# Kernel optimization log

Measured on AMD Instinct MI355X. Metric: run time of the kernel, lower is better.

## Reference

```python
import jax, jax.numpy as jnp
import numpy as np

N, E, NG = 10000, 160000, 64
HID, HEADS = 256, 4
NEG_SLOPE = 0.2


def setup_inputs() -> dict:
    key = jax.random.key(0)
    ks = jax.random.split(key, 20)
    s = 0.1
    inp = {
        "atom_features": jax.random.normal(ks[0], (N, 23), jnp.float32),
        "edge_index": jax.random.randint(ks[1], (2, E), 0, N),
        "batch": jnp.sort(jax.random.randint(ks[2], (N,), 0, NG)),
        "W1": jax.random.normal(ks[3], (23, HEADS * HID), jnp.float32) * s,
        "as1": jax.random.normal(ks[4], (HEADS, HID), jnp.float32) * s,
        "ad1": jax.random.normal(ks[5], (HEADS, HID), jnp.float32) * s,
        "b1": jnp.zeros((HEADS * HID,), jnp.float32),
        "W2": jax.random.normal(ks[6], (HEADS * HID, HEADS * HID), jnp.float32) * s,
        "as2": jax.random.normal(ks[7], (HEADS, HID), jnp.float32) * s,
        "ad2": jax.random.normal(ks[8], (HEADS, HID), jnp.float32) * s,
        "b2": jnp.zeros((HEADS * HID,), jnp.float32),
        "W3": jax.random.normal(ks[9], (HEADS * HID, HID), jnp.float32) * s,
        "as3": jax.random.normal(ks[10], (1, HID), jnp.float32) * s,
        "ad3": jax.random.normal(ks[11], (1, HID), jnp.float32) * s,
        "b3": jnp.zeros((HID,), jnp.float32),
        # MLP head
        "fc1_w": jax.random.normal(ks[12], (HID, HID // 2), jnp.float32) * s,
        "fc1_b": jnp.zeros((HID // 2,), jnp.float32),
        "fc2_w": jax.random.normal(ks[13], (HID // 2, 1), jnp.float32) * s,
        "fc2_b": jnp.zeros((1,), jnp.float32),
    }
    return inp


def gat_layer(x, W, att_src, att_dst, bias, src, dst, heads, ch):
    n = x.shape[0]
    h = (x @ W).reshape(n, heads, ch)                      # [N,H,C]
    a_s = jnp.sum(h * att_src, axis=-1)                    # [N,H]
    a_d = jnp.sum(h * att_dst, axis=-1)                    # [N,H]
    logits = jax.nn.leaky_relu(a_s[src] + a_d[dst], NEG_SLOPE)  # [E',H]
    m = jax.ops.segment_max(logits, dst, num_segments=n)
    m = jnp.where(jnp.isfinite(m), m, 0.0)
    e = jnp.exp(logits - m[dst])
    denom = jax.ops.segment_sum(e, dst, num_segments=n)
    alpha = e / (denom[dst] + 1e-16)                       # segment softmax over incoming edges
    out = jax.ops.segment_sum(alpha[:, :, None] * h[src], dst, num_segments=n)
    return out.reshape(n, heads * ch) + bias


def reference(atom_features, edge_index, batch,
              W1, as1, ad1, b1, W2, as2, ad2, b2, W3, as3, ad3, b3,
              fc1_w, fc1_b, fc2_w, fc2_b):
    n = atom_features.shape[0]
    loops = jnp.arange(n)
    src = jnp.concatenate([edge_index[0], loops])   # PyG GATConv adds self-loops
    dst = jnp.concatenate([edge_index[1], loops])

    x = jax.nn.elu(gat_layer(atom_features, W1, as1, ad1, b1, src, dst, HEADS, HID))
    x = jax.nn.elu(gat_layer(x, W2, as2, ad2, b2, src, dst, HEADS, HID))
    x = jax.nn.elu(gat_layer(x, W3, as3, ad3, b3, src, dst, 1, HID))
    # dropout: eval mode (training=False) -> identity

    # global mean pool over molecules
    sums = jax.ops.segment_sum(x, batch, num_segments=NG)
    counts = jax.ops.segment_sum(jnp.ones((n,), x.dtype), batch, num_segments=NG)
    features = sums / jnp.maximum(counts, 1.0)[:, None]    # [NG, HID]

    hmid = jax.nn.relu(features @ fc1_w + fc1_b)
    validity = hmid @ fc2_w + fc2_b                        # [NG, 1]
    return validity, features
```

## Files before the change

kernel.cpp:

```cpp
#include <hip/hip_runtime.h>
#include <hip/hip_bf16.h>
#include <math.h>

typedef unsigned short ushortT;
typedef __attribute__((ext_vector_type(8))) short short8;
typedef __attribute__((ext_vector_type(4))) float f32x4;

constexpr int NN   = 10000;
constexpr int EE   = 160000;
constexpr int ETOT = EE + NN;
constexpr int NG   = 64;
constexpr int HID  = 256;
constexpr int HEADS = 4;

__device__ __forceinline__ ushortT f2bf(float x) {
    __hip_bfloat16 h = __float2bfloat16(x);
    return *reinterpret_cast<ushortT*>(&h);
}
__device__ __forceinline__ float bf2f(ushortT x) {
    unsigned u = ((unsigned)x) << 16;
    return __uint_as_float(u);
}

__device__ __forceinline__ int xcd_swz(int flat, int nwg) {
    int q = nwg >> 3, r = nwg & 7;
    int xcd = flat & 7, j = flat >> 3;
    return (xcd < r ? xcd * (q + 1) : r * (q + 1) + (xcd - r) * q) + j;
}

__global__ void edge_count_kernel(const int* __restrict__ ei, int* __restrict__ cnt) {
    int e = blockIdx.x * blockDim.x + threadIdx.x;
    if (e >= ETOT) return;
    int dst = (e < EE) ? ei[EE + e] : (e - EE);
    atomicAdd(&cnt[dst], 1);
}

__global__ void scan_kernel(const int* __restrict__ cnt, int* __restrict__ row_ptr,
                            int* __restrict__ cursor) {
    __shared__ int part[256];
    int tid = threadIdx.x;
    const int chunk = (NN + 255) / 256;
    int s0 = tid * chunk;
    int s1 = min(NN, s0 + chunk);
    int sum = 0;
    for (int i = s0; i < s1; ++i) sum += cnt[i];
    part[tid] = sum;
    __syncthreads();
    for (int off = 1; off < 256; off <<= 1) {
        int v = (tid >= off) ? part[tid - off] : 0;
        __syncthreads();
        part[tid] += v;
        __syncthreads();
    }
    int run = (tid == 0) ? 0 : part[tid - 1];
    for (int i = s0; i < s1; ++i) {
        row_ptr[i] = run;
        cursor[i]  = run;
        run += cnt[i];
    }
    if (tid == 255) row_ptr[NN] = part[255];
}

__global__ void edge_fill_kernel(const int* __restrict__ ei, int* __restrict__ cursor,
                                 int* __restrict__ col_src) {
    int e = blockIdx.x * blockDim.x + threadIdx.x;
    if (e >= ETOT) return;
    int src, dst;
    if (e < EE) { src = ei[e]; dst = ei[EE + e]; }
    else        { src = dst = e - EE; }
    int pos = atomicAdd(&cursor[dst], 1);
    col_src[pos] = src;
}

__global__ void convert_wt2(const float* __restrict__ W2, ushortT* __restrict__ wt2,
                            const float* __restrict__ W3, ushortT* __restrict__ wt3) {
    const float* W; ushortT* Wt; int N;
    if (blockIdx.z == 0) { W = W2; Wt = wt2; N = 1024; }
    else                 { W = W3; Wt = wt3; N = 256; if (blockIdx.x >= 8) return; }
    const int K = 1024, Kp = 1024;
    __shared__ float t[32][33];
    int n0 = blockIdx.x * 32, k0 = blockIdx.y * 32;
    int tx = threadIdx.x, ty = threadIdx.y;
    for (int i = ty; i < 32; i += 8) {
        int k = k0 + i, n = n0 + tx;
        t[i][tx] = (k < K && n < N) ? W[(size_t)k * N + n] : 0.f;
    }
    __syncthreads();
    for (int i = ty; i < 32; i += 8) {
        int n = n0 + i, kp = k0 + tx;
        if (n < N && kp < Kp) Wt[(size_t)n * Kp + kp] = f2bf(t[tx][i]);
    }
}

__global__ void build_b1p(const float* __restrict__ W1, ushortT* __restrict__ Bp) {
    int idx = blockIdx.x * 256 + threadIdx.x;
    if (idx >= 1024 * 128) return;
    int n = idx >> 7, kp = idx & 127;
    int h = n >> 8, hk = kp >> 5, k = kp & 31;
    float v = (hk == h && k < 23) ? W1[(size_t)k * 1024 + n] : 0.f;
    Bp[idx] = f2bf(v);
}

__global__ void proj_all(const float* __restrict__ W1, const float* __restrict__ as1,
                         const float* __restrict__ ad1, float* __restrict__ wsv1,
                         const float* __restrict__ W2, const float* __restrict__ as2,
                         const float* __restrict__ ad2, float* __restrict__ wsv2,
                         const float* __restrict__ W3, const float* __restrict__ as3,
                         const float* __restrict__ ad3, float* __restrict__ wsv3) {
    int gw   = (blockIdx.x * 256 + threadIdx.x) >> 6;
    int lane = threadIdx.x & 63;
    const float *W, *atts, *attd; float* wsv; int heads, idx;
    if (gw < 23 * 8)               { W = W1; atts = as1; attd = ad1; wsv = wsv1; heads = 4; idx = gw; }
    else if (gw < 23 * 8 + 8192)   { W = W2; atts = as2; attd = ad2; wsv = wsv2; heads = 4; idx = gw - 184; }
    else if (gw < 23 * 8 + 8192 + 2048) { W = W3; atts = as3; attd = ad3; wsv = wsv3; heads = 1; idx = gw - 184 - 8192; }
    else return;
    const int nout = 2 * heads;
    int k = idx / nout, o = idx - k * nout;
    int h = (o >= heads) ? (o - heads) : o;
    const float* att  = ((o >= heads) ? attd : atts) + h * HID;
    const float* wrow = W + (size_t)k * (heads * HID) + h * HID;
    float4 w4 = *(const float4*)(wrow + lane * 4);
    float4 a4 = *(const float4*)(att + lane * 4);
    float s = w4.x * a4.x + w4.y * a4.y + w4.z * a4.z + w4.w * a4.w;
    #pragma unroll
    for (int off = 1; off < 64; off <<= 1) s += __shfl_xor(s, off);
    if (lane == 0) wsv[(size_t)k * nout + o] = s;
}

__global__ void dots1_kernel(const float* __restrict__ atom,
                             const float* __restrict__ wsv1,
                             float* __restrict__ a_s, float* __restrict__ a_d) {
    int n = blockIdx.x * 256 + threadIdx.x;
    if (n >= NN) return;
    float a[8] = {0.f, 0.f, 0.f, 0.f, 0.f, 0.f, 0.f, 0.f};
    #pragma unroll
    for (int k = 0; k < 23; ++k) {
        float x = atom[n * 23 + k];
        #pragma unroll
        for (int o = 0; o < 8; ++o) a[o] += x * wsv1[k * 8 + o];
    }
    #pragma unroll
    for (int h = 0; h < 4; ++h) { a_s[n * 4 + h] = a[h]; a_d[n * 4 + h] = a[4 + h]; }
}

__global__ void dots2_kernel(const ushortT* __restrict__ x,
                             const float* __restrict__ wsv,
                             float* __restrict__ a_s, float* __restrict__ a_d) {
    int gw = (blockIdx.x * 256 + threadIdx.x) >> 6;
    int lane = threadIdx.x & 63;
    if (gw >= NN) return;
    const ushortT* row = x + (size_t)gw * 1024 + lane * 16;
    short8 v0 = *(const short8*)row;
    short8 v1 = *(const short8*)(row + 8);
    float ps[8] = {0.f, 0.f, 0.f, 0.f, 0.f, 0.f, 0.f, 0.f};
    const float* wb = wsv + (size_t)lane * 16 * 8;
    #pragma unroll
    for (int c = 0; c < 8; ++c) {
        float xv = bf2f((ushortT)v0[c]);
        #pragma unroll
        for (int o = 0; o < 8; ++o) ps[o] += xv * wb[c * 8 + o];
    }
    #pragma unroll
    for (int c = 0; c < 8; ++c) {
        float xv = bf2f((ushortT)v1[c]);
        #pragma unroll
        for (int o = 0; o < 8; ++o) ps[o] += xv * wb[(8 + c) * 8 + o];
    }
    #pragma unroll
    for (int off = 1; off < 64; off <<= 1) {
        #pragma unroll
        for (int o = 0; o < 8; ++o) ps[o] += __shfl_xor(ps[o], off);
    }
    if (lane == 0) {
        #pragma unroll
        for (int h = 0; h < 4; ++h) { a_s[gw * 4 + h] = ps[h]; a_d[gw * 4 + h] = ps[4 + h]; }
    }
}

__global__ void dots3_kernel(const ushortT* __restrict__ x,
                             const float* __restrict__ wsv,
                             float* __restrict__ a_s, float* __restrict__ a_d) {
    int gw = (blockIdx.x * 256 + threadIdx.x) >> 6;
    int lane = threadIdx.x & 63;
    if (gw >= NN) return;
    const ushortT* row = x + (size_t)gw * 1024 + lane * 16;
    short8 v0 = *(const short8*)row;
    short8 v1 = *(const short8*)(row + 8);
    float p0 = 0.f, p1 = 0.f;
    const int c0 = lane * 16;
    #pragma unroll
    for (int c = 0; c < 8; ++c) {
        float xv = bf2f((ushortT)v0[c]);
        float2 w2 = *(const float2*)(wsv + (size_t)(c0 + c) * 2);
        p0 += xv * w2.x; p1 += xv * w2.y;
    }
    #pragma unroll
    for (int c = 0; c < 8; ++c) {
        float xv = bf2f((ushortT)v1[c]);
        float2 w2 = *(const float2*)(wsv + (size_t)(c0 + 8 + c) * 2);
        p0 += xv * w2.x; p1 += xv * w2.y;
    }
    #pragma unroll
    for (int off = 1; off < 64; off <<= 1) {
        p0 += __shfl_xor(p0, off);
        p1 += __shfl_xor(p1, off);
    }
    if (lane == 0) { a_s[gw] = p0; a_d[gw] = p1; }
}

__global__ __launch_bounds__(256) void agg_atom_kernel(const float* __restrict__ atom,
                                                       const float* __restrict__ a_s,
                                                       const float* __restrict__ a_d,
                                                       const int* __restrict__ rowp,
                                                       const int* __restrict__ colv,
                                                       ushortT* __restrict__ Ap) {
    const int wv = threadIdx.x >> 6, lane = threadIdx.x & 63;
    const int i = blockIdx.x * 4 + wv;
    if (i >= NN) return;
    const int half = lane >> 5, c = lane & 31;
    const int start = rowp[i], end = rowp[i + 1];

    __shared__ float wsh[4][64][4];
    __shared__ int   ssh[4][64];

    float acc[4] = {0.f, 0.f, 0.f, 0.f};
    float den4[4] = {0.f, 0.f, 0.f, 0.f};
    for (int cb = start; cb < end; cb += 64) {
        int clen = min(64, end - cb);
        if (lane < clen) {
            int s = colv[cb + lane];
            ssh[wv][lane] = s;
            float4 as4 = *(const float4*)(a_s + (size_t)s * 4);
            float4 ad4 = *(const float4*)(a_d + (size_t)i * 4);
            float l0 = as4.x + ad4.x; l0 = (l0 >= 0.f) ? l0 : 0.2f * l0;
            float l1 = as4.y + ad4.y; l1 = (l1 >= 0.f) ? l1 : 0.2f * l1;
            float l2 = as4.z + ad4.z; l2 = (l2 >= 0.f) ? l2 : 0.2f * l2;
            float l3 = as4.w + ad4.w; l3 = (l3 >= 0.f) ? l3 : 0.2f * l3;
            float w0 = expf(l0), w1 = expf(l1), w2 = expf(l2), w3 = expf(l3);
            *reinterpret_cast<float4*>(&wsh[wv][lane][0]) = make_float4(w0, w1, w2, w3);
            den4[0] += w0; den4[1] += w1; den4[2] += w2; den4[3] += w3;
        }
        __builtin_amdgcn_wave_barrier();
        for (int e = half; e < clen; e += 2) {
            int s = ssh[wv][e];
            float x = (c < 23) ? atom[(size_t)s * 23 + c] : 0.f;
            acc[0] += wsh[wv][e][0] * x;
            acc[1] += wsh[wv][e][1] * x;
            acc[2] += wsh[wv][e][2] * x;
            acc[3] += wsh[wv][e][3] * x;
        }
        __builtin_amdgcn_wave_barrier();
    }
    #pragma unroll
    for (int h = 0; h < 4; ++h) acc[h] += __shfl_xor(acc[h], 32);
    #pragma unroll
    for (int off = 1; off < 64; off <<= 1) {
        den4[0] += __shfl_xor(den4[0], off);
        den4[1] += __shfl_xor(den4[1], off);
        den4[2] += __shfl_xor(den4[2], off);
        den4[3] += __shfl_xor(den4[3], off);
    }
    if (half == 0) {
        #pragma unroll
        for (int h = 0; h < 4; ++h) {
            float v = acc[h] / (den4[h] + 1e-16f);
            Ap[(size_t)i * 128 + h * 32 + c] = f2bf(v);
        }
    }
}

__device__ __forceinline__ void gload_lds16(const ushortT* gsrc, ushortT* ldst) {
    __builtin_amdgcn_global_load_lds(
        (const __attribute__((address_space(1))) unsigned int*)gsrc,
        (__attribute__((address_space(3))) unsigned int*)ldst, 16, 0, 0);
}

template<int MODE>
__global__ __launch_bounds__(256, 2) void gemm_bf16(const ushortT* __restrict__ A,
                                                    const ushortT* __restrict__ Bt,
                                                    ushortT* __restrict__ C,
                                                    const float* __restrict__ bias,
                                                    int M, int N, int K) {
    __shared__ ushortT lds[2][2][128][32];
    const int tid  = threadIdx.x;
    const int lane = tid & 63, w = tid >> 6;
    const int wm = w >> 1, wn = w & 1;
    const int nwg  = gridDim.x * gridDim.y;
    const int flat = blockIdx.y * gridDim.x + blockIdx.x;
    const int swz  = xcd_swz(flat, nwg);
    const int bx = swz % gridDim.x, by = swz / gridDim.x;
    const int row0 = by * 128;
    const int col0 = bx * 128;
    const int nt = K >> 5;

    auto stage = [&](int buf, int t) {
        int k0 = t << 5;
        #pragma unroll
        for (int i = 0; i < 2; ++i) {
            int gbase = (w * 2 + i) * 64;
            int g = gbase + lane;
            int row = g >> 2;
            int sw = (row & 3) ^ ((row >> 2) & 3);
            int koff = (g & 3) ^ sw;
            int arow = min(row0 + row, M - 1);
            gload_lds16(A + (size_t)arow * K + k0 + koff * 8,
                        &lds[buf][0][0][0] + gbase * 8);
            int brow = col0 + row;
            gload_lds16(Bt + (size_t)brow * K + k0 + koff * 8,
                        &lds[buf][1][0][0] + gbase * 8);
        }
    };

    f32x4 acc[4][4] = {};
    const int lr = lane & 15, lk = lane >> 4;

    stage(0, 0);
    for (int t = 0; t < nt; ++t) {
        int buf = t & 1;
        __syncthreads();
        if (t + 1 < nt) stage(buf ^ 1, t + 1);
        short8 a[4], b[4];
        const ushortT* baseA = &lds[buf][0][0][0];
        const ushortT* baseB = &lds[buf][1][0][0];
        #pragma unroll
        for (int m = 0; m < 4; ++m) {
            int row = wm * 64 + m * 16 + lr;
            int sw = (row & 3) ^ ((row >> 2) & 3);
            a[m] = *(const short8*)(baseA + row * 32 + ((lk ^ sw) * 8));
        }
        #pragma unroll
        for (int n = 0; n < 4; ++n) {
            int row = wn * 64 + n * 16 + lr;
            int sw = (row & 3) ^ ((row >> 2) & 3);
            b[n] = *(const short8*)(baseB + row * 32 + ((lk ^ sw) * 8));
        }
        #pragma unroll
        for (int m = 0; m < 4; ++m)
            #pragma unroll
            for (int n = 0; n < 4; ++n)
                acc[m][n] = __builtin_amdgcn_mfma_f32_16x16x32_bf16(a[m], b[n], acc[m][n], 0, 0, 0);
    }

    #pragma unroll
    for (int m = 0; m < 4; ++m) {
        #pragma unroll
        for (int n = 0; n < 4; ++n) {
            int col = col0 + wn * 64 + n * 16 + lr;
            float bv = (MODE == 1) ? bias[col] : 0.f;
            #pragma unroll
            for (int j = 0; j < 4; ++j) {
                int rowg = row0 + wm * 64 + m * 16 + lk * 4 + j;
                if (rowg < M) {
                    float v = acc[m][n][j];
                    if (MODE == 1) { v += bv; v = (v > 0.f) ? v : expm1f(v); }
                    C[(size_t)rowg * N + col] = f2bf(v);
                }
            }
        }
    }
}

__global__ __launch_bounds__(256) void gat_agg_h4(const ushortT* __restrict__ hfeat,
                                                  const float* __restrict__ a_s,
                                                  const float* __restrict__ a_d,
                                                  const int* __restrict__ rowp,
                                                  const int* __restrict__ colv,
                                                  const float* __restrict__ bias,
                                                  ushortT* __restrict__ out16) {
    const int wv = threadIdx.x >> 6, lane = threadIdx.x & 63;
    const int i = blockIdx.x * 4 + wv;
    if (i >= NN) return;
    const int c0 = lane * 16;
    const int hh = c0 >> 8;
    const int start = rowp[i], end = rowp[i + 1];

    __shared__ float wsh[4][64][4];
    __shared__ int   ssh[4][64];

    float acc[16];
    #pragma unroll
    for (int c = 0; c < 16; ++c) acc[c] = 0.f;
    float den4[4] = {0.f, 0.f, 0.f, 0.f};

    for (int cb = start; cb < end; cb += 64) {
        int clen = min(64, end - cb);
        if (lane < clen) {
            int s = colv[cb + lane];
            ssh[wv][lane] = s;
            float4 as4 = *(const float4*)(a_s + (size_t)s * 4);
            float4 ad4 = *(const float4*)(a_d + (size_t)i * 4);
            float l0 = as4.x + ad4.x; l0 = (l0 >= 0.f) ? l0 : 0.2f * l0;
            float l1 = as4.y + ad4.y; l1 = (l1 >= 0.f) ? l1 : 0.2f * l1;
            float l2 = as4.z + ad4.z; l2 = (l2 >= 0.f) ? l2 : 0.2f * l2;
            float l3 = as4.w + ad4.w; l3 = (l3 >= 0.f) ? l3 : 0.2f * l3;
            float w0 = expf(l0), w1 = expf(l1), w2 = expf(l2), w3 = expf(l3);
            *reinterpret_cast<float4*>(&wsh[wv][lane][0]) = make_float4(w0, w1, w2, w3);
            den4[0] += w0; den4[1] += w1; den4[2] += w2; den4[3] += w3;
        }
        __builtin_amdgcn_wave_barrier();
        int e = 0;
        for (; e + 4 <= clen; e += 4) {
            int sa = ssh[wv][e], sb = ssh[wv][e + 1], sc = ssh[wv][e + 2], sd = ssh[wv][e + 3];
            const ushortT* pa = hfeat + (size_t)sa * 1024 + c0;
            const ushortT* pb = hfeat + (size_t)sb * 1024 + c0;
            const ushortT* pc = hfeat + (size_t)sc * 1024 + c0;
            const ushortT* pd = hfeat + (size_t)sd * 1024 + c0;
            short8 va0 = *(const short8*)pa,       va1 = *(const short8*)(pa + 8);
            short8 vb0 = *(const short8*)pb,       vb1 = *(const short8*)(pb + 8);
            short8 vc0 = *(const short8*)pc,       vc1 = *(const short8*)(pc + 8);
            short8 vd0 = *(const short8*)pd,       vd1 = *(const short8*)(pd + 8);
            float wa = wsh[wv][e][hh],     wb = wsh[wv][e + 1][hh];
            float wc = wsh[wv][e + 2][hh], wd = wsh[wv][e + 3][hh];
            #pragma unroll
            for (int j = 0; j < 8; ++j) {
                acc[j]     += wa * bf2f((ushortT)va0[j]) + wb * bf2f((ushortT)vb0[j])
                            + wc * bf2f((ushortT)vc0[j]) + wd * bf2f((ushortT)vd0[j]);
                acc[8 + j] += wa * bf2f((ushortT)va1[j]) + wb * bf2f((ushortT)vb1[j])
                            + wc * bf2f((ushortT)vc1[j]) + wd * bf2f((ushortT)vd1[j]);
            }
        }
        for (; e < clen; ++e) {
            int s = ssh[wv][e];
            float wgt = wsh[wv][e][hh];
            const ushortT* p = hfeat + (size_t)s * 1024 + c0;
            short8 v0 = *(const short8*)p;
            short8 v1 = *(const short8*)(p + 8);
            #pragma unroll
            for (int j = 0; j < 8; ++j) {
                acc[j]     += wgt * bf2f((ushortT)v0[j]);
                acc[8 + j] += wgt * bf2f((ushortT)v1[j]);
            }
        }
        __builtin_amdgcn_wave_barrier();
    }

    #pragma unroll
    for (int off = 1; off < 64; off <<= 1) {
        den4[0] += __shfl_xor(den4[0], off);
        den4[1] += __shfl_xor(den4[1], off);
        den4[2] += __shfl_xor(den4[2], off);
        den4[3] += __shfl_xor(den4[3], off);
    }
    float den = (hh == 0) ? den4[0] : (hh == 1) ? den4[1] : (hh == 2) ? den4[2] : den4[3];
    float inv = 1.f / (den + 1e-16f);

    ushortT pk[16];
    #pragma unroll
    for (int c = 0; c < 16; ++c) {
        float v = acc[c] * inv + bias[c0 + c];
        v = (v > 0.f) ? v : expm1f(v);
        pk[c] = f2bf(v);
    }
    *reinterpret_cast<short8*>(out16 + (size_t)i * 1024 + c0)     = *reinterpret_cast<short8*>(&pk[0]);
    *reinterpret_cast<short8*>(out16 + (size_t)i * 1024 + c0 + 8) = *reinterpret_cast<short8*>(&pk[8]);
}

__global__ __launch_bounds__(256) void gat_agg_h1(const ushortT* __restrict__ hfeat,
                                                  const float* __restrict__ a_s,
                                                  const float* __restrict__ a_d,
                                                  const int* __restrict__ rowp,
                                                  const int* __restrict__ colv,
                                                  const float* __restrict__ bias,
                                                  float* __restrict__ outf) {
    const int wv = threadIdx.x >> 6, lane = threadIdx.x & 63;
    const int i = blockIdx.x * 4 + wv;
    if (i >= NN) return;
    const int c0 = lane * 4;
    const int start = rowp[i], end = rowp[i + 1];
    const float adi = a_d[i];

    __shared__ float wsh[4][64];
    __shared__ int   ssh[4][64];

    float acc[4] = {0.f, 0.f, 0.f, 0.f};
    float den = 0.f;

    for (int cb = start; cb < end; cb += 64) {
        int clen = min(64, end - cb);
        if (lane < clen) {
            int s = colv[cb + lane];
            ssh[wv][lane] = s;
            float l = a_s[s] + adi;
            l = (l >= 0.f) ? l : 0.2f * l;
            float w0 = expf(l);
            wsh[wv][lane] = w0;
            den += w0;
        }
        __builtin_amdgcn_wave_barrier();
        int e = 0;
        for (; e + 4 <= clen; e += 4) {
            int sa = ssh[wv][e], sb = ssh[wv][e + 1], sc = ssh[wv][e + 2], sd = ssh[wv][e + 3];
            ushort4 va = *(const ushort4*)(hfeat + (size_t)sa * 256 + c0);
            ushort4 vb = *(const ushort4*)(hfeat + (size_t)sb * 256 + c0);
            ushort4 vc = *(const ushort4*)(hfeat + (size_t)sc * 256 + c0);
            ushort4 vd = *(const ushort4*)(hfeat + (size_t)sd * 256 + c0);
            float wa = wsh[wv][e], wb2 = wsh[wv][e + 1], wc2 = wsh[wv][e + 2], wd2 = wsh[wv][e + 3];
            acc[0] += wa * bf2f(va.x) + wb2 * bf2f(vb.x) + wc2 * bf2f(vc.x) + wd2 * bf2f(vd.x);
            acc[1] += wa * bf2f(va.y) + wb2 * bf2f(vb.y) + wc2 * bf2f(vc.y) + wd2 * bf2f(vd.y);
            acc[2] += wa * bf2f(va.z) + wb2 * bf2f(vb.z) + wc2 * bf2f(vc.z) + wd2 * bf2f(vd.z);
            acc[3] += wa * bf2f(va.w) + wb2 * bf2f(vb.w) + wc2 * bf2f(vc.w) + wd2 * bf2f(vd.w);
        }
        for (; e < clen; ++e) {
            int s = ssh[wv][e];
            float wgt = wsh[wv][e];
            ushort4 v = *(const ushort4*)(hfeat + (size_t)s * 256 + c0);
            acc[0] += wgt * bf2f(v.x); acc[1] += wgt * bf2f(v.y);
            acc[2] += wgt * bf2f(v.z); acc[3] += wgt * bf2f(v.w);
        }
        __builtin_amdgcn_wave_barrier();
    }

    #pragma unroll
    for (int off = 1; off < 64; off <<= 1) den += __shfl_xor(den, off);
    float inv = 1.f / (den + 1e-16f);

    float4 o4;
    float v0 = acc[0] * inv + bias[c0 + 0]; o4.x = (v0 > 0.f) ? v0 : expm1f(v0);
    float v1 = acc[1] * inv + bias[c0 + 1]; o4.y = (v1 > 0.f) ? v1 : expm1f(v1);
    float v2 = acc[2] * inv + bias[c0 + 2]; o4.z = (v2 > 0.f) ? v2 : expm1f(v2);
    float v3 = acc[3] * inv + bias[c0 + 3]; o4.w = (v3 > 0.f) ? v3 : expm1f(v3);
    *reinterpret_cast<float4*>(outf + (size_t)i * 256 + c0) = o4;
}

__global__ void pool_mlp(const float* __restrict__ x,
                         const int* __restrict__ batch,
                         const float* __restrict__ fc1_w,
                         const float* __restrict__ fc1_b,
                         const float* __restrict__ fc2_w,
                         const float* __restrict__ fc2_b,
                         float* __restrict__ out) {
    int g = blockIdx.x, tid = threadIdx.x;
    int lo = 0, hi = NN;
    while (lo < hi) { int mid = (lo + hi) >> 1; if (batch[mid] < g) lo = mid + 1; else hi = mid; }
    int s0 = lo;
    lo = 0; hi = NN;
    while (lo < hi) { int mid = (lo + hi) >> 1; if (batch[mid] < g + 1) lo = mid + 1; else hi = mid; }
    int s1 = lo;

    float acc = 0.f;
    for (int n = s0; n < s1; ++n) acc += x[(size_t)n * HID + tid];
    float cnt = (float)(s1 - s0);
    float feat = acc / fmaxf(cnt, 1.f);
    out[NG + g * HID + tid] = feat;

    __shared__ float fsh[HID];
    fsh[tid] = feat;
    __syncthreads();
    __shared__ float r2[128];
    if (tid < 128) {
        float a = fc1_b[tid];
        for (int c = 0; c < HID; ++c) a += fsh[c] * fc1_w[c * 128 + tid];
        a = fmaxf(a, 0.f);
        r2[tid] = a * fc2_w[tid];
    }
    __syncthreads();
    for (int s2 = 64; s2 > 0; s2 >>= 1) {
        if (tid < s2) r2[tid] += r2[tid + s2];
        __syncthreads();
    }
    if (tid == 0) out[g] = r2[0] + fc2_b[0];
}

extern "C" void kernel_launch(void* const* d_in, const int* in_sizes, int n_in,
                              void* d_out, int out_size, void* d_ws, size_t ws_size,
                              hipStream_t stream) {
    const float* atom  = (const float*)d_in[0];
    const int*   ei    = (const int*)  d_in[1];
    const int*   batch = (const int*)  d_in[2];
    const float* W1  = (const float*)d_in[3];
    const float* as1 = (const float*)d_in[4];
    const float* ad1 = (const float*)d_in[5];
    const float* b1  = (const float*)d_in[6];
    const float* W2  = (const float*)d_in[7];
    const float* as2 = (const float*)d_in[8];
    const float* ad2 = (const float*)d_in[9];
    const float* b2  = (const float*)d_in[10];
    const float* W3  = (const float*)d_in[11];
    const float* as3 = (const float*)d_in[12];
    const float* ad3 = (const float*)d_in[13];
    const float* b3  = (const float*)d_in[14];
    const float* fc1w = (const float*)d_in[15];
    const float* fc1b = (const float*)d_in[16];
    const float* fc2w = (const float*)d_in[17];
    const float* fc2b = (const float*)d_in[18];
    float* out = (float*)d_out;

    ushortT* h16  = (ushortT*)d_ws;
    ushortT* x16  = h16 + (size_t)NN * 1024;
    ushortT* Ap   = x16 + (size_t)NN * 1024;
    ushortT* b1p  = Ap + (size_t)NN * 128;
    ushortT* wt2  = b1p + 1024 * 128;
    ushortT* wt3  = wt2 + 1024 * 1024;
    float*   x3   = (float*)(wt3 + 256 * 1024);
    float*   asL1 = x3 + (size_t)NN * 256;
    float*   adL1 = asL1 + (size_t)NN * 4;
    float*   asL2 = adL1 + (size_t)NN * 4;
    float*   adL2 = asL2 + (size_t)NN * 4;
    float*   asL3 = adL2 + (size_t)NN * 4;
    float*   adL3 = asL3 + NN;
    float*   wsv1 = adL3 + NN;
    float*   wsv2 = wsv1 + 23 * 8;
    float*   wsv3 = wsv2 + 1024 * 8;
    int*   cnt    = (int*)(wsv3 + 1024 * 2);
    int*   rowp   = cnt + NN;
    int*   cursor = rowp + NN + 1;
    int*   col    = cursor + NN;

    hipMemsetAsync(cnt, 0, NN * sizeof(int), stream);
    edge_count_kernel<<<(ETOT + 255) / 256, 256, 0, stream>>>(ei, cnt);
    scan_kernel<<<1, 256, 0, stream>>>(cnt, rowp, cursor);
    edge_fill_kernel<<<(ETOT + 255) / 256, 256, 0, stream>>>(ei, cursor, col);

    convert_wt2<<<dim3(32, 32, 2), dim3(32, 8), 0, stream>>>(W2, wt2, W3, wt3);
    build_b1p<<<(1024 * 128 + 255) / 256, 256, 0, stream>>>(W1, b1p);
    proj_all<<<((23 * 8 + 8192 + 2048) * 64 + 255) / 256, 256, 0, stream>>>(
        W1, as1, ad1, wsv1, W2, as2, ad2, wsv2, W3, as3, ad3, wsv3);

    dim3 blk(256);
    const int gy   = (NN + 127) / 128;
    const int gagg = (NN + 3) / 4;

    dots1_kernel<<<(NN + 255) / 256, blk, 0, stream>>>(atom, wsv1, asL1, adL1);
    agg_atom_kernel<<<gagg, blk, 0, stream>>>(atom, asL1, adL1, rowp, col, Ap);
    gemm_bf16<1><<<dim3(8, gy), blk, 0, stream>>>(Ap, b1p, x16, b1, NN, 1024, 128);

    dots2_kernel<<<gagg, blk, 0, stream>>>(x16, wsv2, asL2, adL2);
    gemm_bf16<0><<<dim3(8, gy), blk, 0, stream>>>(x16, wt2, h16, nullptr, NN, 1024, 1024);
    gat_agg_h4<<<gagg, blk, 0, stream>>>(h16, asL2, adL2, rowp, col, b2, x16);

    dots3_kernel<<<gagg, blk, 0, stream>>>(x16, wsv3, asL3, adL3);
    gemm_bf16<0><<<dim3(2, gy), blk, 0, stream>>>(x16, wt3, h16, nullptr, NN, 256, 1024);
    gat_agg_h1<<<gagg, blk, 0, stream>>>(h16, asL3, adL3, rowp, col, b3, x3);

    pool_mlp<<<NG, blk, 0, stream>>>(x3, batch, fc1w, fc1b, fc2w, fc2b, out);
}
```

Before: 324.1 us.

## Merge setup, fill/dots1, and dots into GEMM launches via block-range dispatch

Combines weight conversion, W1 packing, attention projection and the count memset into one setup kernel. Merges edge fill with the layer-1 attention dots, and appends the layer-2/3 attention dot work as extra blocks in the same launch as the corresponding GEMM. This cuts the number of kernel launches and the serial gaps between small kernels, letting the light dot blocks fill idle CUs alongside the GEMM tiles. In exchange, the shared LDS allocation and register pressure of the GEMM branch now apply to the dot blocks too, which can lower their occupancy.

```diff
diff --git a/kernel.cpp b/kernel.cpp
--- a/kernel.cpp
+++ b/kernel.cpp
@@ -26,6 +26,63 @@
     int q = nwg >> 3, r = nwg & 7;
     int xcd = flat & 7, j = flat >> 3;
     return (xcd < r ? xcd * (q + 1) : r * (q + 1) + (xcd - r) * q) + j;
+}
+
+__global__ __launch_bounds__(256) void setup_kernel(
+        const float* __restrict__ W1, const float* __restrict__ as1,
+        const float* __restrict__ ad1, float* __restrict__ wsv1,
+        const float* __restrict__ W2, const float* __restrict__ as2,
+        const float* __restrict__ ad2, float* __restrict__ wsv2,
+        const float* __restrict__ W3, const float* __restrict__ as3,
+        const float* __restrict__ ad3, float* __restrict__ wsv3,
+        ushortT* __restrict__ wt2, ushortT* __restrict__ wt3,
+        ushortT* __restrict__ b1p, int* __restrict__ cnt) {
+    __shared__ float t[32][33];
+    const int b = blockIdx.x, tid = threadIdx.x;
+    if (b < 1280) {
+        const float* W; ushortT* Wt; int N, n0, k0;
+        if (b < 1024) { W = W2; Wt = wt2; N = 1024; n0 = (b & 31) * 32; k0 = (b >> 5) * 32; }
+        else          { int b2 = b - 1024; W = W3; Wt = wt3; N = 256; n0 = (b2 & 7) * 32; k0 = (b2 >> 3) * 32; }
+        const int K = 1024, Kp = 1024;
+        int tx = tid & 31, ty = tid >> 5;
+        for (int i = ty; i < 32; i += 8) {
+            int k = k0 + i, n = n0 + tx;
+            t[i][tx] = (k < K && n < N) ? W[(size_t)k * N + n] : 0.f;
+        }
+        __syncthreads();
+        for (int i = ty; i < 32; i += 8) {
+            int n = n0 + i, kp = k0 + tx;
+            if (n < N && kp < Kp) Wt[(size_t)n * Kp + kp] = f2bf(t[tx][i]);
+        }
+    } else if (b < 1792) {
+        int idx = (b - 1280) * 256 + tid;
+        int n = idx >> 7, kp = idx & 127;
+        int h = n >> 8, hk = kp >> 5, k = kp & 31;
+        float v = (hk == h && k < 23) ? W1[(size_t)k * 1024 + n] : 0.f;
+        b1p[idx] = f2bf(v);
+    } else if (b < 4398) {
+        int gw = (b - 1792) * 4 + (tid >> 6);
+        int lane = tid & 63;
+        const float *W, *atts, *attd; float* wsv; int heads, idx;
+        if (gw < 184)            { W = W1; atts = as1; attd = ad1; wsv = wsv1; heads = 4; idx = gw; }
+        else if (gw < 184 + 8192){ W = W2; atts = as2; attd = ad2; wsv = wsv2; heads = 4; idx = gw - 184; }
+        else if (gw < 184 + 8192 + 2048) { W = W3; atts = as3; attd = ad3; wsv = wsv3; heads = 1; idx = gw - 184 - 8192; }
+        else return;
+        const int nout = 2 * heads;
+        int k = idx / nout, o = idx - k * nout;
+        int h = (o >= heads) ? (o - heads) : o;
+        const float* att  = ((o >= heads) ? attd : atts) + h * HID;
+        const float* wrow = W + (size_t)k * (heads * HID) + h * HID;
+        float4 w4 = *(const float4*)(wrow + lane * 4);
+        float4 a4 = *(const float4*)(att + lane * 4);
+        float s = w4.x * a4.x + w4.y * a4.y + w4.z * a4.z + w4.w * a4.w;
+        #pragma unroll
+        for (int off = 1; off < 64; off <<= 1) s += __shfl_xor(s, off);
+        if (lane == 0) wsv[(size_t)k * nout + o] = s;
+    } else {
+        int idx = (b - 4398) * 256 + tid;
+        if (idx < NN) cnt[idx] = 0;
+    }
 }
 
 __global__ void edge_count_kernel(const int* __restrict__ ei, int* __restrict__ cnt) {
@@ -61,151 +118,34 @@
     if (tid == 255) row_ptr[NN] = part[255];
 }
 
-__global__ void edge_fill_kernel(const int* __restrict__ ei, int* __restrict__ cursor,
-                                 int* __restrict__ col_src) {
-    int e = blockIdx.x * blockDim.x + threadIdx.x;
-    if (e >= ETOT) return;
-    int src, dst;
-    if (e < EE) { src = ei[e]; dst = ei[EE + e]; }
-    else        { src = dst = e - EE; }
-    int pos = atomicAdd(&cursor[dst], 1);
-    col_src[pos] = src;
-}
-
-__global__ void convert_wt2(const float* __restrict__ W2, ushortT* __restrict__ wt2,
-                            const float* __restrict__ W3, ushortT* __restrict__ wt3) {
-    const float* W; ushortT* Wt; int N;
-    if (blockIdx.z == 0) { W = W2; Wt = wt2; N = 1024; }
-    else                 { W = W3; Wt = wt3; N = 256; if (blockIdx.x >= 8) return; }
-    const int K = 1024, Kp = 1024;
-    __shared__ float t[32][33];
-    int n0 = blockIdx.x * 32, k0 = blockIdx.y * 32;
-    int tx = threadIdx.x, ty = threadIdx.y;
-    for (int i = ty; i < 32; i += 8) {
-        int k = k0 + i, n = n0 + tx;
-        t[i][tx] = (k < K && n < N) ? W[(size_t)k * N + n] : 0.f;
-    }
-    __syncthreads();
-    for (int i = ty; i < 32; i += 8) {
-        int n = n0 + i, kp = k0 + tx;
-        if (n < N && kp < Kp) Wt[(size_t)n * Kp + kp] = f2bf(t[tx][i]);
-    }
-}
-
-__global__ void build_b1p(const float* __restrict__ W1, ushortT* __restrict__ Bp) {
-    int idx = blockIdx.x * 256 + threadIdx.x;
-    if (idx >= 1024 * 128) return;
-    int n = idx >> 7, kp = idx & 127;
-    int h = n >> 8, hk = kp >> 5, k = kp & 31;
-    float v = (hk == h && k < 23) ? W1[(size_t)k * 1024 + n] : 0.f;
-    Bp[idx] = f2bf(v);
-}
-
-__global__ void proj_all(const float* __restrict__ W1, const float* __restrict__ as1,
-                         const float* __restrict__ ad1, float* __restrict__ wsv1,
-                         const float* __restrict__ W2, const float* __restrict__ as2,
-                         const float* __restrict__ ad2, float* __restrict__ wsv2,
-                         const float* __restrict__ W3, const float* __restrict__ as3,
-                         const float* __restrict__ ad3, float* __restrict__ wsv3) {
-    int gw   = (blockIdx.x * 256 + threadIdx.x) >> 6;
-    int lane = threadIdx.x & 63;
-    const float *W, *atts, *attd; float* wsv; int heads, idx;
-    if (gw < 23 * 8)               { W = W1; atts = as1; attd = ad1; wsv = wsv1; heads = 4; idx = gw; }
-    else if (gw < 23 * 8 + 8192)   { W = W2; atts = as2; attd = ad2; wsv = wsv2; heads = 4; idx = gw - 184; }
-    else if (gw < 23 * 8 + 8192 + 2048) { W = W3; atts = as3; attd = ad3; wsv = wsv3; heads = 1; idx = gw - 184 - 8192; }
-    else return;
-    const int nout = 2 * heads;
-    int k = idx / nout, o = idx - k * nout;
-    int h = (o >= heads) ? (o - heads) : o;
-    const float* att  = ((o >= heads) ? attd : atts) + h * HID;
-    const float* wrow = W + (size_t)k * (heads * HID) + h * HID;
-    float4 w4 = *(const float4*)(wrow + lane * 4);
-    float4 a4 = *(const float4*)(att + lane * 4);
-    float s = w4.x * a4.x + w4.y * a4.y + w4.z * a4.z + w4.w * a4.w;
-    #pragma unroll
-    for (int off = 1; off < 64; off <<= 1) s += __shfl_xor(s, off);
-    if (lane == 0) wsv[(size_t)k * nout + o] = s;
-}
-
-__global__ void dots1_kernel(const float* __restrict__ atom,
-                             const float* __restrict__ wsv1,
-                             float* __restrict__ a_s, float* __restrict__ a_d) {
-    int n = blockIdx.x * 256 + threadIdx.x;
-    if (n >= NN) return;
-    float a[8] = {0.f, 0.f, 0.f, 0.f, 0.f, 0.f, 0.f, 0.f};
-    #pragma unroll
-    for (int k = 0; k < 23; ++k) {
-        float x = atom[n * 23 + k];
-        #pragma unroll
-        for (int o = 0; o < 8; ++o) a[o] += x * wsv1[k * 8 + o];
-    }
-    #pragma unroll
-    for (int h = 0; h < 4; ++h) { a_s[n * 4 + h] = a[h]; a_d[n * 4 + h] = a[4 + h]; }
-}
-
-__global__ void dots2_kernel(const ushortT* __restrict__ x,
-                             const float* __restrict__ wsv,
-                             float* __restrict__ a_s, float* __restrict__ a_d) {
-    int gw = (blockIdx.x * 256 + threadIdx.x) >> 6;
-    int lane = threadIdx.x & 63;
-    if (gw >= NN) return;
-    const ushortT* row = x + (size_t)gw * 1024 + lane * 16;
-    short8 v0 = *(const short8*)row;
-    short8 v1 = *(const short8*)(row + 8);
-    float ps[8] = {0.f, 0.f, 0.f, 0.f, 0.f, 0.f, 0.f, 0.f};
-    const float* wb = wsv + (size_t)lane * 16 * 8;
-    #pragma unroll
-    for (int c = 0; c < 8; ++c) {
-        float xv = bf2f((ushortT)v0[c]);
-        #pragma unroll
-        for (int o = 0; o < 8; ++o) ps[o] += xv * wb[c * 8 + o];
-    }
-    #pragma unroll
-    for (int c = 0; c < 8; ++c) {
-        float xv = bf2f((ushortT)v1[c]);
-        #pragma unroll
-        for (int o = 0; o < 8; ++o) ps[o] += xv * wb[(8 + c) * 8 + o];
-    }
-    #pragma unroll
-    for (int off = 1; off < 64; off <<= 1) {
-        #pragma unroll
-        for (int o = 0; o < 8; ++o) ps[o] += __shfl_xor(ps[o], off);
-    }
-    if (lane == 0) {
-        #pragma unroll
-        for (int h = 0; h < 4; ++h) { a_s[gw * 4 + h] = ps[h]; a_d[gw * 4 + h] = ps[4 + h]; }
-    }
-}
-
-__global__ void dots3_kernel(const ushortT* __restrict__ x,
-                             const float* __restrict__ wsv,
-                             float* __restrict__ a_s, float* __restrict__ a_d) {
-    int gw = (blockIdx.x * 256 + threadIdx.x) >> 6;
-    int lane = threadIdx.x & 63;
-    if (gw >= NN) return;
-    const ushortT* row = x + (size_t)gw * 1024 + lane * 16;
-    short8 v0 = *(const short8*)row;
-    short8 v1 = *(const short8*)(row + 8);
-    float p0 = 0.f, p1 = 0.f;
-    const int c0 = lane * 16;
-    #pragma unroll
-    for (int c = 0; c < 8; ++c) {
-        float xv = bf2f((ushortT)v0[c]);
-        float2 w2 = *(const float2*)(wsv + (size_t)(c0 + c) * 2);
-        p0 += xv * w2.x; p1 += xv * w2.y;
-    }
-    #pragma unroll
-    for (int c = 0; c < 8; ++c) {
-        float xv = bf2f((ushortT)v1[c]);
-        float2 w2 = *(const float2*)(wsv + (size_t)(c0 + 8 + c) * 2);
-        p0 += xv * w2.x; p1 += xv * w2.y;
-    }
-    #pragma unroll
-    for (int off = 1; off < 64; off <<= 1) {
-        p0 += __shfl_xor(p0, off);
-        p1 += __shfl_xor(p1, off);
-    }
-    if (lane == 0) { a_s[gw] = p0; a_d[gw] = p1; }
+__global__ void fill_dots1_kernel(const int* __restrict__ ei, int* __restrict__ cursor,
+                                  int* __restrict__ col_src,
+                                  const float* __restrict__ atom,
+                                  const float* __restrict__ wsv1,
+                                  float* __restrict__ a_s, float* __restrict__ a_d,
+                                  int nfill) {
+    int b = blockIdx.x;
+    if (b < nfill) {
+        int e = b * 256 + threadIdx.x;
+        if (e >= ETOT) return;
+        int src, dst;
+        if (e < EE) { src = ei[e]; dst = ei[EE + e]; }
+        else        { src = dst = e - EE; }
+        int pos = atomicAdd(&cursor[dst], 1);
+        col_src[pos] = src;
+    } else {
+        int n = (b - nfill) * 256 + threadIdx.x;
+        if (n >= NN) return;
+        float a[8] = {0.f, 0.f, 0.f, 0.f, 0.f, 0.f, 0.f, 0.f};
+        #pragma unroll
+        for (int k = 0; k < 23; ++k) {
+            float x = atom[n * 23 + k];
+            #pragma unroll
+            for (int o = 0; o < 8; ++o) a[o] += x * wsv1[k * 8 + o];
+        }
+        #pragma unroll
+        for (int h = 0; h < 4; ++h) { a_s[n * 4 + h] = a[h]; a_d[n * 4 + h] = a[4 + h]; }
+    }
 }
 
 __global__ __launch_bounds__(256) void agg_atom_kernel(const float* __restrict__ atom,
@@ -275,88 +215,149 @@
         (__attribute__((address_space(3))) unsigned int*)ldst, 16, 0, 0);
 }
 
-template<int MODE>
-__global__ __launch_bounds__(256, 2) void gemm_bf16(const ushortT* __restrict__ A,
-                                                    const ushortT* __restrict__ Bt,
-                                                    ushortT* __restrict__ C,
-                                                    const float* __restrict__ bias,
-                                                    int M, int N, int K) {
-    __shared__ ushortT lds[2][2][128][32];
-    const int tid  = threadIdx.x;
-    const int lane = tid & 63, w = tid >> 6;
-    const int wm = w >> 1, wn = w & 1;
-    const int nwg  = gridDim.x * gridDim.y;
-    const int flat = blockIdx.y * gridDim.x + blockIdx.x;
-    const int swz  = xcd_swz(flat, nwg);
-    const int bx = swz % gridDim.x, by = swz / gridDim.x;
-    const int row0 = by * 128;
-    const int col0 = bx * 128;
-    const int nt = K >> 5;
-
-    auto stage = [&](int buf, int t) {
-        int k0 = t << 5;
-        #pragma unroll
-        for (int i = 0; i < 2; ++i) {
-            int gbase = (w * 2 + i) * 64;
-            int g = gbase + lane;
-            int row = g >> 2;
-            int sw = (row & 3) ^ ((row >> 2) & 3);
-            int koff = (g & 3) ^ sw;
-            int arow = min(row0 + row, M - 1);
-            gload_lds16(A + (size_t)arow * K + k0 + koff * 8,
-                        &lds[buf][0][0][0] + gbase * 8);
-            int brow = col0 + row;
-            gload_lds16(Bt + (size_t)brow * K + k0 + koff * 8,
-                        &lds[buf][1][0][0] + gbase * 8);
-        }
-    };
-
-    f32x4 acc[4][4] = {};
-    const int lr = lane & 15, lk = lane >> 4;
-
-    stage(0, 0);
-    for (int t = 0; t < nt; ++t) {
-        int buf = t & 1;
-        __syncthreads();
-        if (t + 1 < nt) stage(buf ^ 1, t + 1);
-        short8 a[4], b[4];
-        const ushortT* baseA = &lds[buf][0][0][0];
-        const ushortT* baseB = &lds[buf][1][0][0];
+template<int MODE, int DOTS>
+__global__ __launch_bounds__(256, 2) void gemm_fused(const ushortT* __restrict__ A,
+                                                     const ushortT* __restrict__ Bt,
+                                                     ushortT* __restrict__ C,
+                                                     const float* __restrict__ bias,
+                                                     const float* __restrict__ wsv,
+                                                     float* __restrict__ da_s,
+                                                     float* __restrict__ da_d,
+                                                     int M, int N, int K,
+                                                     int nx, int ngemm) {
+    if ((int)blockIdx.x < ngemm) {
+        __shared__ ushortT lds[2][2][128][32];
+        const int tid  = threadIdx.x;
+        const int lane = tid & 63, w = tid >> 6;
+        const int wm = w >> 1, wn = w & 1;
+        const int swz  = xcd_swz(blockIdx.x, ngemm);
+        const int bx = swz % nx, by = swz / nx;
+        const int row0 = by * 128;
+        const int col0 = bx * 128;
+        const int nt = K >> 5;
+
+        auto stage = [&](int buf, int t) {
+            int k0 = t << 5;
+            #pragma unroll
+            for (int i = 0; i < 2; ++i) {
+                int gbase = (w * 2 + i) * 64;
+                int g = gbase + lane;
+                int row = g >> 2;
+                int sw = (row & 3) ^ ((row >> 2) & 3);
+                int koff = (g & 3) ^ sw;
+                int arow = min(row0 + row, M - 1);
+                gload_lds16(A + (size_t)arow * K + k0 + koff * 8,
+                            &lds[buf][0][0][0] + gbase * 8);
+                int brow = col0 + row;
+                gload_lds16(Bt + (size_t)brow * K + k0 + koff * 8,
+                            &lds[buf][1][0][0] + gbase * 8);
+            }
+        };
+
+        f32x4 acc[4][4] = {};
+        const int lr = lane & 15, lk = lane >> 4;
+
+        stage(0, 0);
+        for (int t = 0; t < nt; ++t) {
+            int buf = t & 1;
+            __syncthreads();
+            if (t + 1 < nt) stage(buf ^ 1, t + 1);
+            short8 a[4], b[4];
+            const ushortT* baseA = &lds[buf][0][0][0];
+            const ushortT* baseB = &lds[buf][1][0][0];
+            #pragma unroll
+            for (int m = 0; m < 4; ++m) {
+                int row = wm * 64 + m * 16 + lr;
+                int sw = (row & 3) ^ ((row >> 2) & 3);
+                a[m] = *(const short8*)(baseA + row * 32 + ((lk ^ sw) * 8));
+            }
+            #pragma unroll
+            for (int n = 0; n < 4; ++n) {
+                int row = wn * 64 + n * 16 + lr;
+                int sw = (row & 3) ^ ((row >> 2) & 3);
+                b[n] = *(const short8*)(baseB + row * 32 + ((lk ^ sw) * 8));
+            }
+            #pragma unroll
+            for (int m = 0; m < 4; ++m)
+                #pragma unroll
+                for (int n = 0; n < 4; ++n)
+                    acc[m][n] = __builtin_amdgcn_mfma_f32_16x16x32_bf16(a[m], b[n], acc[m][n], 0, 0, 0);
+        }
+
         #pragma unroll
         for (int m = 0; m < 4; ++m) {
-            int row = wm * 64 + m * 16 + lr;
-            int sw = (row & 3) ^ ((row >> 2) & 3);
-            a[m] = *(const short8*)(baseA + row * 32 + ((lk ^ sw) * 8));
-        }
-        #pragma unroll
-        for (int n = 0; n < 4; ++n) {
-            int row = wn * 64 + n * 16 + lr;
-            int sw = (row & 3) ^ ((row >> 2) & 3);
-            b[n] = *(const short8*)(baseB + row * 32 + ((lk ^ sw) * 8));
-        }
-        #pragma unroll
-        for (int m = 0; m < 4; ++m)
-            #pragma unroll
-            for (int n = 0; n < 4; ++n)
-                acc[m][n] = __builtin_amdgcn_mfma_f32_16x16x32_bf16(a[m], b[n], acc[m][n], 0, 0, 0);
-    }
-
-    #pragma unroll
-    for (int m = 0; m < 4; ++m) {
-        #pragma unroll
-        for (int n = 0; n < 4; ++n) {
-            int col = col0 + wn * 64 + n * 16 + lr;
-            float bv = (MODE == 1) ? bias[col] : 0.f;
-            #pragma unroll
-            for (int j = 0; j < 4; ++j) {
-                int rowg = row0 + wm * 64 + m * 16 + lk * 4 + j;
-                if (rowg < M) {
-                    float v = acc[m][n][j];
-                    if (MODE == 1) { v += bv; v = (v > 0.f) ? v : expm1f(v); }
-                    C[(size_t)rowg * N + col] = f2bf(v);
+            #pragma unroll
+            for (int n = 0; n < 4; ++n) {
+                int col = col0 + wn * 64 + n * 16 + lr;
+                float bv = (MODE == 1) ? bias[col] : 0.f;
+                #pragma unroll
+                for (int j = 0; j < 4; ++j) {
+                    int rowg = row0 + wm * 64 + m * 16 + lk * 4 + j;
+                    if (rowg < M) {
+                        float v = acc[m][n][j];
+                        if (MODE == 1) { v += bv; v = (v > 0.f) ? v : expm1f(v); }
+                        C[(size_t)rowg * N + col] = f2bf(v);
+                    }
                 }
             }
         }
+    } else if (DOTS == 2) {
+        int gw = ((int)blockIdx.x - ngemm) * 4 + (threadIdx.x >> 6);
+        int lane = threadIdx.x & 63;
+        if (gw >= NN) return;
+        const ushortT* row = A + (size_t)gw * 1024 + lane * 16;
+        short8 v0 = *(const short8*)row;
+        short8 v1 = *(const short8*)(row + 8);
+        float ps[8] = {0.f, 0.f, 0.f, 0.f, 0.f, 0.f, 0.f, 0.f};
+        const float* wb = wsv + (size_t)lane * 16 * 8;
+        #pragma unroll
+        for (int c = 0; c < 8; ++c) {
+            float xv = bf2f((ushortT)v0[c]);
+            #pragma unroll
+            for (int o = 0; o < 8; ++o) ps[o] += xv * wb[c * 8 + o];
+        }
+        #pragma unroll
+        for (int c = 0; c < 8; ++c) {
+            float xv = bf2f((ushortT)v1[c]);
+            #pragma unroll
+            for (int o = 0; o < 8; ++o) ps[o] += xv * wb[(8 + c) * 8 + o];
+        }
+        #pragma unroll
+        for (int off = 1; off < 64; off <<= 1) {
+            #pragma unroll
+            for (int o = 0; o < 8; ++o) ps[o] += __shfl_xor(ps[o], off);
+        }
+        if (lane == 0) {
+            #pragma unroll
+            for (int h = 0; h < 4; ++h) { da_s[gw * 4 + h] = ps[h]; da_d[gw * 4 + h] = ps[4 + h]; }
+        }
+    } else if (DOTS == 3) {
+        int gw = ((int)blockIdx.x - ngemm) * 4 + (threadIdx.x >> 6);
+        int lane = threadIdx.x & 63;
+        if (gw >= NN) return;
+        const ushortT* row = A + (size_t)gw * 1024 + lane * 16;
+        short8 v0 = *(const short8*)row;
+        short8 v1 = *(const short8*)(row + 8);
+        float p0 = 0.f, p1 = 0.f;
+        const int c0 = lane * 16;
+        #pragma unroll
+        for (int c = 0; c < 8; ++c) {
+            float xv = bf2f((ushortT)v0[c]);
+            float2 w2 = *(const float2*)(wsv + (size_t)(c0 + c) * 2);
+            p0 += xv * w2.x; p1 += xv * w2.y;
+        }
+        #pragma unroll
+        for (int c = 0; c < 8; ++c) {
+            float xv = bf2f((ushortT)v1[c]);
+            float2 w2 = *(const float2*)(wsv + (size_t)(c0 + 8 + c) * 2);
+            p0 += xv * w2.x; p1 += xv * w2.y;
+        }
+        #pragma unroll
+        for (int off = 1; off < 64; off <<= 1) {
+            p0 += __shfl_xor(p0, off);
+            p1 += __shfl_xor(p1, off);
+        }
+        if (lane == 0) { da_s[gw] = p0; da_d[gw] = p1; }
     }
 }
 
@@ -606,30 +607,29 @@
     int*   cursor = rowp + NN + 1;
     int*   col    = cursor + NN;
 
-    hipMemsetAsync(cnt, 0, NN * sizeof(int), stream);
-    edge_count_kernel<<<(ETOT + 255) / 256, 256, 0, stream>>>(ei, cnt);
-    scan_kernel<<<1, 256, 0, stream>>>(cnt, rowp, cursor);
-    edge_fill_kernel<<<(ETOT + 255) / 256, 256, 0, stream>>>(ei, cursor, col);
-
-    convert_wt2<<<dim3(32, 32, 2), dim3(32, 8), 0, stream>>>(W2, wt2, W3, wt3);
-    build_b1p<<<(1024 * 128 + 255) / 256, 256, 0, stream>>>(W1, b1p);
-    proj_all<<<((23 * 8 + 8192 + 2048) * 64 + 255) / 256, 256, 0, stream>>>(
-        W1, as1, ad1, wsv1, W2, as2, ad2, wsv2, W3, as3, ad3, wsv3);
-
     dim3 blk(256);
+    const int gagg = (NN + 3) / 4;
     const int gy   = (NN + 127) / 128;
-    const int gagg = (NN + 3) / 4;
-
-    dots1_kernel<<<(NN + 255) / 256, blk, 0, stream>>>(atom, wsv1, asL1, adL1);
+
+    setup_kernel<<<4438, blk, 0, stream>>>(W1, as1, ad1, wsv1, W2, as2, ad2, wsv2,
+                                           W3, as3, ad3, wsv3, wt2, wt3, b1p, cnt);
+
+    edge_count_kernel<<<(ETOT + 255) / 256, blk, 0, stream>>>(ei, cnt);
+    scan_kernel<<<1, blk, 0, stream>>>(cnt, rowp, cursor);
+    const int nfill = (ETOT + 255) / 256;
+    fill_dots1_kernel<<<nfill + (NN + 255) / 256, blk, 0, stream>>>(
+        ei, cursor, col, atom, wsv1, asL1, adL1, nfill);
+
     agg_atom_kernel<<<gagg, blk, 0, stream>>>(atom, asL1, adL1, rowp, col, Ap);
-    gemm_bf16<1><<<dim3(8, gy), blk, 0, stream>>>(Ap, b1p, x16, b1, NN, 1024, 128);
-
-    dots2_kernel<<<gagg, blk, 0, stream>>>(x16, wsv2, asL2, adL2);
-    gemm_bf16<0><<<dim3(8, gy), blk, 0, stream>>>(x16, wt2, h16, nullptr, NN, 1024, 1024);
+    gemm_fused<1, 0><<<8 * gy, blk, 0, stream>>>(Ap, b1p, x16, b1, nullptr, nullptr, nullptr,
+                                                 NN, 1024, 128, 8, 8 * gy);
+
+    gemm_fused<0, 2><<<8 * gy + gagg, blk, 0, stream>>>(x16, wt2, h16, nullptr, wsv2,
+                                                        asL2, adL2, NN, 1024, 1024, 8, 8 * gy);
     gat_agg_h4<<<gagg, blk, 0, stream>>>(h16, asL2, adL2, rowp, col, b2, x16);
 
-    dots3_kernel<<<gagg, blk, 0, stream>>>(x16, wsv3, asL3, adL3);
-    gemm_bf16<0><<<dim3(2, gy), blk, 0, stream>>>(x16, wt3, h16, nullptr, NN, 256, 1024);
+    gemm_fused<0, 3><<<2 * gy + gagg, blk, 0, stream>>>(x16, wt3, h16, nullptr, wsv3,
+                                                        asL3, adL3, NN, 256, 1024, 2, 2 * gy);
     gat_agg_h1<<<gagg, blk, 0, stream>>>(h16, asL3, adL3, rowp, col, b3, x3);
 
     pool_mlp<<<NG, blk, 0, stream>>>(x3, batch, fc1w, fc1b, fc2w, fc2b, out);
```

After: 300.8 us. 7.2% less time.
